# Kernel tuning notes

Measured on AMD Instinct MI355X. Metric: run time of the kernel, lower is better.

The kernel has to match this reference:

```python
import jax, jax.numpy as jnp
import numpy as np

V, E, D = 50000, 800000, 128
EH, NH = 128, 128  # edge_hidden, node_hidden


def setup_inputs() -> dict:
    key = jax.random.key(0)
    ks = jax.random.split(key, 12)
    h = jax.random.normal(ks[0], (V, D), dtype=jnp.float32)
    edge_index = jax.random.randint(ks[1], (2, E), 0, V, dtype=jnp.int64)
    s = 0.02
    # edge MLP: Linear(2D->EH), Linear(EH->EH), Linear(EH->NH)
    W1 = jax.random.normal(ks[2], (2 * D, EH), dtype=jnp.float32) * s
    b1 = jnp.zeros((EH,), dtype=jnp.float32)
    W2 = jax.random.normal(ks[3], (EH, EH), dtype=jnp.float32) * s
    b2 = jnp.zeros((EH,), dtype=jnp.float32)
    W3 = jax.random.normal(ks[4], (EH, NH), dtype=jnp.float32) * s
    b3 = jnp.zeros((NH,), dtype=jnp.float32)
    # node MLP: Linear(D+NH->NH), Linear(NH->NH)
    Wn1 = jax.random.normal(ks[5], (D + NH, NH), dtype=jnp.float32) * s
    bn1 = jnp.zeros((NH,), dtype=jnp.float32)
    Wn2 = jax.random.normal(ks[6], (NH, NH), dtype=jnp.float32) * s
    bn2 = jnp.zeros((NH,), dtype=jnp.float32)
    return {"h": h, "edge_index": edge_index, "W1": W1, "b1": b1, "W2": W2,
            "b2": b2, "W3": W3, "b3": b3, "Wn1": Wn1, "bn1": bn1,
            "Wn2": Wn2, "bn2": bn2}


def reference(h, edge_index, W1, b1, W2, b2, W3, b3, Wn1, bn1, Wn2, bn2):
    src, dst = edge_index[0], edge_index[1]
    # gather node pairs -> edge features (E, 2D)
    edge_feat = jnp.concatenate([h[src], h[dst]], axis=-1)
    # 3-layer edge MLP
    m = jax.nn.relu(edge_feat @ W1 + b1)
    m = jax.nn.relu(m @ W2 + b2)
    messages = m @ W3 + b3                       # (E, NH)
    # scatter-add into destination nodes
    agg = jax.ops.segment_sum(messages, dst, num_segments=h.shape[0])  # (V, NH)
    # node MLP on [h, agg]
    x = jnp.concatenate([h, agg], axis=-1)       # (V, D+NH)
    out = jax.nn.relu(x @ Wn1 + bn1) @ Wn2 + bn2  # (V, NH)
    return out
```

## Files before the change

### kernel.cpp

```cpp
#include <hip/hip_runtime.h>

#define NV 50000
#define NE 800000
#define CVT_N 1600000
#define TR_N  81920
#define W3N_N 16384
#define B3N_N 128
#define NB1 49

typedef _Float16 f16x8 __attribute__((ext_vector_type(8)));
typedef _Float16 f16x4 __attribute__((ext_vector_type(4)));
typedef float    f32x4 __attribute__((ext_vector_type(4)));

static __device__ __forceinline__ f32x4 mfma16(f16x8 a, f16x8 b, f32x4 c) {
  return __builtin_amdgcn_mfma_f32_16x16x32_f16(a, b, c, 0, 0, 0);
}

__global__ void prep_kernel(const float* __restrict__ h, _Float16* __restrict__ hf,
    const float* __restrict__ W1, const float* __restrict__ W2, const float* __restrict__ W3,
    const float* __restrict__ Wn1, const float* __restrict__ Wn2, const float* __restrict__ b3,
    _Float16* __restrict__ w1st, _Float16* __restrict__ w1dt, _Float16* __restrict__ w2t,
    _Float16* __restrict__ wn1c, _Float16* __restrict__ wn2t, float* __restrict__ b3n,
    const int* __restrict__ ei, int* __restrict__ counts)
{
  int i = blockIdx.x * blockDim.x + threadIdx.x;
  if (i < CVT_N) {
    f32x4 v = reinterpret_cast<const f32x4*>(h)[i];
    f16x4 o;
    o[0] = (_Float16)v[0]; o[1] = (_Float16)v[1]; o[2] = (_Float16)v[2]; o[3] = (_Float16)v[3];
    reinterpret_cast<f16x4*>(hf)[i] = o;
    return;
  }
  i -= CVT_N;
  if (i < TR_N) {
    int seg = i >> 14;
    int j = i & 16383;
    int f = j >> 7, k = j & 127;
    switch (seg) {
      case 0: w1st[j] = (_Float16)W1[k * 128 + f]; break;
      case 1: w1dt[j] = (_Float16)W1[(k + 128) * 128 + f]; break;
      case 2: w2t[j]  = (_Float16)W2[k * 128 + f]; break;
      case 3: wn1c[f * 256 + k] = (_Float16)Wn1[k * 128 + f]; break;
      case 4: wn2t[j] = (_Float16)Wn2[k * 128 + f]; break;
    }
    return;
  }
  i -= TR_N;
  if (i < W3N_N) {
    int f = i >> 7, ii = i & 127;
    float a = 0.f;
    for (int j = 0; j < 128; j++) a += W3[ii * 128 + j] * Wn1[(128 + j) * 128 + f];
    wn1c[f * 256 + 128 + ii] = (_Float16)a;
    return;
  }
  i -= W3N_N;
  if (i < B3N_N) {
    float a = 0.f;
    for (int j = 0; j < 128; j++) a += b3[j] * Wn1[(128 + j) * 128 + i];
    b3n[i] = a;
    return;
  }
  i -= B3N_N;
  if (i < NE) atomicAdd(&counts[ei[NE + i]], 1);
}

__global__ __launch_bounds__(1024)
void bsum_kernel(const int* __restrict__ counts, int* __restrict__ bsum) {
  __shared__ int red[1024];
  const int t = threadIdx.x;
  int i = blockIdx.x * 1024 + t;
  red[t] = (i < NV) ? counts[i] : 0;
  __syncthreads();
  for (int off = 512; off > 0; off >>= 1) {
    if (t < off) red[t] += red[t + off];
    __syncthreads();
  }
  if (t == 0) bsum[blockIdx.x] = red[0];
}

__global__ void bscan_kernel(const int* __restrict__ bsum, int* __restrict__ boff) {
  if (threadIdx.x == 0 && blockIdx.x == 0) {
    int run = 0;
    for (int b = 0; b < NB1; b++) { boff[b] = run; run += bsum[b]; }
    boff[NB1] = run;
  }
}

__global__ __launch_bounds__(1024)
void offs_kernel(const int* __restrict__ counts, const int* __restrict__ boff,
                 int* __restrict__ offsets, int* __restrict__ cursor) {
  __shared__ int s[1024];
  const int t = threadIdx.x;
  int i = blockIdx.x * 1024 + t;
  int v = (i < NV) ? counts[i] : 0;
  s[t] = v;
  __syncthreads();
  for (int off = 1; off < 1024; off <<= 1) {
    int x = (t >= off) ? s[t - off] : 0;
    __syncthreads();
    s[t] += x;
    __syncthreads();
  }
  if (i < NV) {
    int excl = boff[blockIdx.x] + s[t] - v;
    offsets[i] = excl;
    cursor[i] = excl;
    if (i == NV - 1) offsets[NV] = boff[blockIdx.x] + s[t];
  }
}

__global__ void permute_kernel(const int* __restrict__ ei, int* __restrict__ cursor,
                               int2* __restrict__ pairs) {
  int e = blockIdx.x * blockDim.x + threadIdx.x;
  if (e < NE) {
    int s = ei[e], d = ei[NE + e];
    int pos = atomicAdd(&cursor[d], 1);
    pairs[pos] = make_int2(s, d);
  }
}

static __device__ __forceinline__ void gemm128_rows(
    const _Float16* __restrict__ hf, const int* nid, const _Float16* __restrict__ At,
    const float* __restrict__ bias, _Float16* __restrict__ Out,
    int nbase, int l15, int quad)
{
  f32x4 acc[8][4];
#pragma unroll
  for (int mt = 0; mt < 8; mt++)
#pragma unroll
    for (int nt = 0; nt < 4; nt++)
      acc[mt][nt] = (f32x4){0.f, 0.f, 0.f, 0.f};

  f16x8 Bc[4], Bn[4];
#pragma unroll
  for (int nt = 0; nt < 4; nt++)
    Bc[nt] = *reinterpret_cast<const f16x8*>(hf + (long long)nid[nt] * 128 + quad * 8);
#pragma unroll
  for (int s = 0; s < 4; s++) {
    if (s < 3) {
#pragma unroll
      for (int nt = 0; nt < 4; nt++)
        Bn[nt] = *reinterpret_cast<const f16x8*>(hf + (long long)nid[nt] * 128 + (s + 1) * 32 + quad * 8);
    }
    const int k = s * 32 + quad * 8;
#pragma unroll
    for (int mt = 0; mt < 8; mt++) {
      f16x8 A = *reinterpret_cast<const f16x8*>(At + (mt * 16 + l15) * 128 + k);
#pragma unroll
      for (int nt = 0; nt < 4; nt++)
        acc[mt][nt] = mfma16(A, Bc[nt], acc[mt][nt]);
    }
#pragma unroll
    for (int nt = 0; nt < 4; nt++) Bc[nt] = Bn[nt];
  }
#pragma unroll
  for (int mt = 0; mt < 8; mt++) {
    f32x4 bb = bias ? *reinterpret_cast<const f32x4*>(bias + mt * 16 + quad * 4)
                    : (f32x4){0.f, 0.f, 0.f, 0.f};
#pragma unroll
    for (int nt = 0; nt < 4; nt++) {
      int n = nbase + nt * 16 + l15;
      if (n < NV) {
        f16x4 o;
#pragma unroll
        for (int r = 0; r < 4; r++) o[r] = (_Float16)(acc[mt][nt][r] + bb[r]);
        *reinterpret_cast<f16x4*>(Out + (long long)n * 128 + mt * 16 + quad * 4) = o;
      }
    }
  }
}

__global__ __launch_bounds__(256, 2)
void h1_kernel(const _Float16* __restrict__ hf, const float* __restrict__ b1,
               const _Float16* __restrict__ w1st, const _Float16* __restrict__ w1dt,
               _Float16* __restrict__ H1s, _Float16* __restrict__ H1d)
{
  const int t = threadIdx.x;
  const int lane = t & 63, wave = t >> 6;
  const int quad = lane >> 4, l15 = lane & 15;
  const int nbase = blockIdx.x * 256 + wave * 64;
  int nid[4];
#pragma unroll
  for (int nt = 0; nt < 4; nt++) {
    int n = nbase + nt * 16 + l15;
    nid[nt] = n < NV ? n : NV - 1;
  }
  if (blockIdx.y == 0) gemm128_rows(hf, nid, w1st, nullptr, H1s, nbase, l15, quad);
  else                 gemm128_rows(hf, nid, w1dt, b1,      H1d, nbase, l15, quad);
}

__global__ __launch_bounds__(128, 3)
void edge_kernel(const _Float16* __restrict__ H1s, const _Float16* __restrict__ H1d,
                 const int2* __restrict__ pairs,
                 const _Float16* __restrict__ w2t, const float* __restrict__ b2,
                 float* __restrict__ agg2)
{
  __shared__ __align__(16) _Float16 M2t[64 * 128];
  __shared__ int segdst[128];
  __shared__ __align__(8) unsigned char sseg8[128];
  __shared__ unsigned long long wmask[2];
  __shared__ int sopen[2];

  const int t = threadIdx.x;
  const int lane = t & 63, wave = t >> 6;
  const int quad = lane >> 4, l15 = lane & 15;
  const int ebase = blockIdx.x * 128;
  const int wbase = wave * 64;

  const int2 prt = pairs[ebase + t];
  if (t == 0)   sopen[0] = (ebase > 0) && (prt.y == pairs[ebase - 1].y);
  if (t == 127) sopen[1] = (ebase + 128 < NE) && (prt.y == pairs[ebase + 128].y);
  const int dprev = (t > 0) ? pairs[ebase + t - 1].y : -1;

  int esrc[4], edst[4];
#pragma unroll
  for (int et = 0; et < 4; et++) {
    int2 pr = pairs[ebase + wbase + et * 16 + l15];
    esrc[et] = pr.x; edst[et] = pr.y;
  }

  f16x8 m1f[4][4];
#pragma unroll
  for (int et = 0; et < 4; et++) {
#pragma unroll
    for (int s = 0; s < 4; s++) {
      f16x8 a = *reinterpret_cast<const f16x8*>(H1s + (long long)esrc[et] * 128 + s * 32 + quad * 8);
      f16x8 b = *reinterpret_cast<const f16x8*>(H1d + (long long)edst[et] * 128 + s * 32 + quad * 8);
      f16x8 o = a + b;
#pragma unroll
      for (int j = 0; j < 8; j++) o[j] = o[j] > (_Float16)0 ? o[j] : (_Float16)0;
      m1f[et][s] = o;
    }
  }

  const bool flag = (t > 0) && (prt.y != dprev);
  unsigned long long bm = __ballot(flag);
  if (lane == 0) wmask[wave] = bm;
  int pre = __popcll(bm & ((1ull << lane) - 1ull)) + (flag ? 1 : 0);
  __syncthreads();
  const int sid = pre + (wave ? (int)__popcll(wmask[0]) : 0);
  sseg8[t] = (unsigned char)sid;
  if (flag || t == 0) segdst[sid] = prt.y;
  const int nseg = (int)__popcll(wmask[0]) + (int)__popcll(wmask[1]) + 1;
  const int nmt = (nseg + 15) >> 4;
  const bool openL = sopen[0] != 0;
  const bool openR = sopen[1] != 0;

  for (int half = 0; half < 2; half++) {
    f32x4 acc[4][4];
#pragma unroll
    for (int et = 0; et < 4; et++)
#pragma unroll
      for (int ft = 0; ft < 4; ft++)
        acc[et][ft] = (f32x4){0.f, 0.f, 0.f, 0.f};

#pragma unroll
    for (int s = 0; s < 4; s++) {
      const int k = s * 32 + quad * 8;
#pragma unroll
      for (int ft = 0; ft < 4; ft++) {
        f16x8 B = *reinterpret_cast<const f16x8*>(w2t + ((half * 4 + ft) * 16 + l15) * 128 + k);
#pragma unroll
        for (int et = 0; et < 4; et++)
          acc[et][ft] = mfma16(m1f[et][s], B, acc[et][ft]);
      }
    }
#pragma unroll
    for (int ft = 0; ft < 4; ft++) {
      const float bv = b2[(half * 4 + ft) * 16 + l15];
#pragma unroll
      for (int et = 0; et < 4; et++) {
        const int g = wave * 16 + et * 4 + quad;
        f16x4 o;
#pragma unroll
        for (int r = 0; r < 4; r++) {
          float x = acc[et][ft][r] + bv;
          o[r] = (_Float16)(x > 0.f ? x : 0.f);
        }
        *reinterpret_cast<f16x4*>(&M2t[(ft * 16 + l15) * 128 + ((g ^ (l15 << 1)) * 4)]) = o;
      }
    }
    __syncthreads();

    f16x8 Bf[2][4];
#pragma unroll
    for (int fl = 0; fl < 2; fl++) {
      const int flr = (wave * 2 + fl) * 16 + l15;
#pragma unroll
      for (int s = 0; s < 4; s++) {
        const int g0 = s * 8 + quad * 2;
        Bf[fl][s] = *reinterpret_cast<const f16x8*>(&M2t[flr * 128 + ((g0 ^ (l15 << 1)) * 4)]);
      }
    }
    unsigned long long segb[4];
#pragma unroll
    for (int s = 0; s < 4; s++)
      segb[s] = *reinterpret_cast<const unsigned long long*>(&sseg8[s * 32 + quad * 8]);
    __syncthreads();

    for (int mt = 0; mt < nmt; mt++) {
      const int myseg = mt * 16 + l15;
      f32x4 racc[2];
#pragma unroll
      for (int fl = 0; fl < 2; fl++) racc[fl] = (f32x4){0.f, 0.f, 0.f, 0.f};
#pragma unroll
      for (int s = 0; s < 4; s++) {
        f16x8 S;
#pragma unroll
        for (int j = 0; j < 8; j++)
          S[j] = ((int)((segb[s] >> (8 * j)) & 255ull) == myseg) ? (_Float16)1 : (_Float16)0;
#pragma unroll
        for (int fl = 0; fl < 2; fl++)
          racc[fl] = mfma16(S, Bf[fl][s], racc[fl]);
      }
#pragma unroll
      for (int fl = 0; fl < 2; fl++) {
        const int f = half * 64 + (wave * 2 + fl) * 16 + l15;
#pragma unroll
        for (int r = 0; r < 4; r++) {
          const int sg = mt * 16 + quad * 4 + r;
          if (sg < nseg) {
            float v = racc[fl][r];
            float* p = agg2 + (long long)segdst[sg] * 128 + f;
            const bool at = (sg == 0 && openL) || (sg == nseg - 1 && openR);
            if (at) unsafeAtomicAdd(p, v); else *p = v;
          }
        }
      }
    }
  }
}

__global__ __launch_bounds__(256, 2)
void node_kernel(const _Float16* __restrict__ hf, const float* __restrict__ agg2,
                 const int* __restrict__ offsets,
                 const _Float16* __restrict__ wn1c, const float* __restrict__ bn1,
                 const float* __restrict__ b3n,
                 const _Float16* __restrict__ wn2t, const float* __restrict__ bn2,
                 float* __restrict__ out)
{
  __shared__ __align__(16) _Float16 M[256 * 128];
  const int t = threadIdx.x;
  const int lane = t & 63, wave = t >> 6;
  const int quad = lane >> 4, l15 = lane & 15;
  const int wbase = wave * 64;
  const int nbase = blockIdx.x * 256 + wbase;

  int nid[4]; float fcnt[4];
#pragma unroll
  for (int nt = 0; nt < 4; nt++) {
    int n = nbase + nt * 16 + l15;
    nid[nt] = n < NV ? n : NV - 1;
    fcnt[nt] = (n < NV) ? (float)(offsets[n + 1] - offsets[n]) : 0.f;
  }

  f32x4 acc[8][4];
#pragma unroll
  for (int mt = 0; mt < 8; mt++)
#pragma unroll
    for (int nt = 0; nt < 4; nt++)
      acc[mt][nt] = (f32x4){0.f, 0.f, 0.f, 0.f};

  f16x8 Bc[4], Bn[4];
#pragma unroll
  for (int nt = 0; nt < 4; nt++)
    Bc[nt] = *reinterpret_cast<const f16x8*>(hf + (long long)nid[nt] * 128 + quad * 8);
#pragma unroll
  for (int s = 0; s < 8; s++) {
    if (s < 7) {
      const int sn = s + 1;
      if (sn < 4) {
#pragma unroll
        for (int nt = 0; nt < 4; nt++)
          Bn[nt] = *reinterpret_cast<const f16x8*>(hf + (long long)nid[nt] * 128 + sn * 32 + quad * 8);
      } else {
#pragma unroll
        for (int nt = 0; nt < 4; nt++) {
          const float* ap = agg2 + (long long)nid[nt] * 128 + (sn - 4) * 32 + quad * 8;
          f32x4 a0 = *reinterpret_cast<const f32x4*>(ap);
          f32x4 a1 = *reinterpret_cast<const f32x4*>(ap + 4);
          f16x8 bb;
#pragma unroll
          for (int j = 0; j < 4; j++) { bb[j] = (_Float16)a0[j]; bb[4 + j] = (_Float16)a1[j]; }
          Bn[nt] = bb;
        }
      }
    }
    const int k = s * 32 + quad * 8;
#pragma unroll
    for (int mt = 0; mt < 8; mt++) {
      f16x8 A = *reinterpret_cast<const f16x8*>(wn1c + (mt * 16 + l15) * 256 + k);
#pragma unroll
      for (int nt = 0; nt < 4; nt++)
        acc[mt][nt] = mfma16(A, Bc[nt], acc[mt][nt]);
    }
#pragma unroll
    for (int nt = 0; nt < 4; nt++) Bc[nt] = Bn[nt];
  }
#pragma unroll
  for (int mt = 0; mt < 8; mt++) {
    f32x4 bb  = *reinterpret_cast<const f32x4*>(bn1 + mt * 16 + quad * 4);
    f32x4 b3c = *reinterpret_cast<const f32x4*>(b3n + mt * 16 + quad * 4);
    const int cbase = 2 * mt + (quad >> 1);
#pragma unroll
    for (int nt = 0; nt < 4; nt++) {
      int row = wbase + nt * 16 + l15;
      int c = cbase ^ (row & 15);
      f16x4 o;
#pragma unroll
      for (int r = 0; r < 4; r++) {
        float x = acc[mt][nt][r] + bb[r] + fcnt[nt] * b3c[r];
        o[r] = (_Float16)(x > 0.f ? x : 0.f);
      }
      *reinterpret_cast<f16x4*>(&M[row * 128 + c * 8 + (quad & 1) * 4]) = o;
      acc[mt][nt] = (f32x4){0.f, 0.f, 0.f, 0.f};
    }
  }

#pragma unroll
  for (int s = 0; s < 4; s++) {
    f16x8 B[4];
#pragma unroll
    for (int nt = 0; nt < 4; nt++) {
      int row = wbase + nt * 16 + l15;
      B[nt] = *reinterpret_cast<const f16x8*>(&M[row * 128 + (((4 * s + quad) ^ (row & 15)) * 8)]);
    }
    const int k = s * 32 + quad * 8;
#pragma unroll
    for (int mt = 0; mt < 8; mt++) {
      f16x8 A = *reinterpret_cast<const f16x8*>(wn2t + (mt * 16 + l15) * 128 + k);
#pragma unroll
      for (int nt = 0; nt < 4; nt++)
        acc[mt][nt] = mfma16(A, B[nt], acc[mt][nt]);
    }
  }
#pragma unroll
  for (int mt = 0; mt < 8; mt++) {
    f32x4 bias = *reinterpret_cast<const f32x4*>(bn2 + mt * 16 + quad * 4);
#pragma unroll
    for (int nt = 0; nt < 4; nt++) {
      int n = nbase + nt * 16 + l15;
      if (n < NV) {
        f32x4 v;
#pragma unroll
        for (int r = 0; r < 4; r++) v[r] = acc[mt][nt][r] + bias[r];
        *reinterpret_cast<f32x4*>(out + (long long)n * 128 + mt * 16 + quad * 4) = v;
      }
    }
  }
}

static inline size_t align16(size_t x) { return (x + 15) & ~(size_t)15; }

extern "C" void kernel_launch(void* const* d_in, const int* in_sizes, int n_in,
                              void* d_out, int out_size, void* d_ws, size_t ws_size,
                              hipStream_t stream)
{
  const float* h   = (const float*)d_in[0];
  const int*   ei  = (const int*)d_in[1];
  const float* W1  = (const float*)d_in[2];
  const float* b1  = (const float*)d_in[3];
  const float* W2  = (const float*)d_in[4];
  const float* b2  = (const float*)d_in[5];
  const float* W3  = (const float*)d_in[6];
  const float* b3  = (const float*)d_in[7];
  const float* Wn1 = (const float*)d_in[8];
  const float* bn1 = (const float*)d_in[9];
  const float* Wn2 = (const float*)d_in[10];
  const float* bn2 = (const float*)d_in[11];
  float* out = (float*)d_out;

  char* p = (char*)d_ws;
  _Float16* hf   = (_Float16*)p; p += align16((size_t)NV * 128 * 2);
  _Float16* H1s  = (_Float16*)p; p += align16((size_t)NV * 128 * 2);
  _Float16* H1d  = (_Float16*)p; p += align16((size_t)NV * 128 * 2);
  _Float16* w1st = (_Float16*)p; p += align16(128 * 128 * 2);
  _Float16* w1dt = (_Float16*)p; p += align16(128 * 128 * 2);
  _Float16* w2t  = (_Float16*)p; p += align16(128 * 128 * 2);
  _Float16* wn1c = (_Float16*)p; p += align16(128 * 256 * 2);
  _Float16* wn2t = (_Float16*)p; p += align16(128 * 128 * 2);
  float*  b3n  = (float*)p;  p += align16(128 * 4);
  int* counts  = (int*)p; p += align16((size_t)NV * 4);
  int* offsets = (int*)p; p += align16((size_t)(NV + 1) * 4);
  int* cursor  = (int*)p; p += align16((size_t)NV * 4);
  int* bsum    = (int*)p; p += align16((size_t)(NB1 + 1) * 4);
  int* boff    = (int*)p; p += align16((size_t)(NB1 + 1) * 4);
  int2* pairs  = (int2*)p; p += align16((size_t)NE * 8);
  float* agg2  = (float*)p; p += align16((size_t)NV * 128 * 4);

  hipMemsetAsync(counts, 0, (size_t)NV * 4, stream);
  hipMemsetAsync(agg2, 0, (size_t)NV * 128 * 4, stream);
  {
    int total = CVT_N + TR_N + W3N_N + B3N_N + NE;
    prep_kernel<<<(total + 255) / 256, 256, 0, stream>>>(
        h, hf, W1, W2, W3, Wn1, Wn2, b3,
        w1st, w1dt, w2t, wn1c, wn2t, b3n, ei, counts);
  }
  bsum_kernel<<<NB1, 1024, 0, stream>>>(counts, bsum);
  bscan_kernel<<<1, 64, 0, stream>>>(bsum, boff);
  offs_kernel<<<NB1, 1024, 0, stream>>>(counts, boff, offsets, cursor);
  permute_kernel<<<(NE + 255) / 256, 256, 0, stream>>>(ei, cursor, pairs);
  h1_kernel<<<dim3((NV + 255) / 256, 2), 256, 0, stream>>>(hf, b1, w1st, w1dt, H1s, H1d);
  edge_kernel<<<NE / 128, 128, 0, stream>>>(H1s, H1d, pairs, w2t, b2, agg2);
  node_kernel<<<(NV + 255) / 256, 256, 0, stream>>>(hf, agg2, offsets, wn1c, bn1, b3n,
                                                    wn2t, bn2, out);
}
```

Measured before the change: 385.7 us.

## Fold block scan into offsets kernel and merge permute with H1 GEMM launch

Removes the single-thread bscan kernel by having each offsets block compute its base with a wave reduction over bsum. It also merges the edge permutation and the H1 GEMM into one launch using block-index partitioning, so the atomic scatter and the MFMA work can run side by side. In edge_kernel, segment-boundary detection now goes through a shared-memory dst array instead of extra global loads, and launch_bounds min-blocks drops from 3 to 2. The aim is fewer launches and better overlap, at the cost of a mixed-workload kernel and possibly lower edge-kernel occupancy.

```diff
diff --git a/kernel.cpp b/kernel.cpp
--- a/kernel.cpp
+++ b/kernel.cpp
@@ -7,6 +7,8 @@
 #define W3N_N 16384
 #define B3N_N 128
 #define NB1 49
+#define NB_PERM 3125
+#define NB_H1 196
 
 typedef _Float16 f16x8 __attribute__((ext_vector_type(8)));
 typedef _Float16 f16x4 __attribute__((ext_vector_type(4)));
@@ -78,22 +80,20 @@
   if (t == 0) bsum[blockIdx.x] = red[0];
 }
 
-__global__ void bscan_kernel(const int* __restrict__ bsum, int* __restrict__ boff) {
-  if (threadIdx.x == 0 && blockIdx.x == 0) {
-    int run = 0;
-    for (int b = 0; b < NB1; b++) { boff[b] = run; run += bsum[b]; }
-    boff[NB1] = run;
-  }
-}
-
 __global__ __launch_bounds__(1024)
-void offs_kernel(const int* __restrict__ counts, const int* __restrict__ boff,
+void offs_kernel(const int* __restrict__ counts, const int* __restrict__ bsum,
                  int* __restrict__ offsets, int* __restrict__ cursor) {
   __shared__ int s[1024];
+  __shared__ int sbase;
   const int t = threadIdx.x;
   int i = blockIdx.x * 1024 + t;
   int v = (i < NV) ? counts[i] : 0;
   s[t] = v;
+  if (t < 64) {
+    int x = (t < blockIdx.x) ? bsum[t] : 0;
+    for (int off = 1; off < 64; off <<= 1) x += __shfl_xor(x, off);
+    if (t == 0) sbase = x;
+  }
   __syncthreads();
   for (int off = 1; off < 1024; off <<= 1) {
     int x = (t >= off) ? s[t - off] : 0;
@@ -102,20 +102,10 @@
     __syncthreads();
   }
   if (i < NV) {
-    int excl = boff[blockIdx.x] + s[t] - v;
+    int excl = sbase + s[t] - v;
     offsets[i] = excl;
     cursor[i] = excl;
-    if (i == NV - 1) offsets[NV] = boff[blockIdx.x] + s[t];
-  }
-}
-
-__global__ void permute_kernel(const int* __restrict__ ei, int* __restrict__ cursor,
-                               int2* __restrict__ pairs) {
-  int e = blockIdx.x * blockDim.x + threadIdx.x;
-  if (e < NE) {
-    int s = ei[e], d = ei[NE + e];
-    int pos = atomicAdd(&cursor[d], 1);
-    pairs[pos] = make_int2(s, d);
+    if (i == NV - 1) offsets[NV] = sbase + s[t];
   }
 }
 
@@ -171,35 +161,49 @@
 }
 
 __global__ __launch_bounds__(256, 2)
-void h1_kernel(const _Float16* __restrict__ hf, const float* __restrict__ b1,
-               const _Float16* __restrict__ w1st, const _Float16* __restrict__ w1dt,
-               _Float16* __restrict__ H1s, _Float16* __restrict__ H1d)
+void h1p_kernel(const _Float16* __restrict__ hf, const float* __restrict__ b1,
+                const _Float16* __restrict__ w1st, const _Float16* __restrict__ w1dt,
+                _Float16* __restrict__ H1s, _Float16* __restrict__ H1d,
+                const int* __restrict__ ei, int* __restrict__ cursor,
+                int2* __restrict__ pairs)
 {
+  int bx = blockIdx.x;
+  if (bx < NB_PERM) {
+    int e = bx * 256 + threadIdx.x;
+    int s = ei[e], d = ei[NE + e];
+    int pos = atomicAdd(&cursor[d], 1);
+    pairs[pos] = make_int2(s, d);
+    return;
+  }
+  bx -= NB_PERM;
+  const int by = bx & 1;
+  const int bxx = bx >> 1;
   const int t = threadIdx.x;
   const int lane = t & 63, wave = t >> 6;
   const int quad = lane >> 4, l15 = lane & 15;
-  const int nbase = blockIdx.x * 256 + wave * 64;
+  const int nbase = bxx * 256 + wave * 64;
   int nid[4];
 #pragma unroll
   for (int nt = 0; nt < 4; nt++) {
     int n = nbase + nt * 16 + l15;
     nid[nt] = n < NV ? n : NV - 1;
   }
-  if (blockIdx.y == 0) gemm128_rows(hf, nid, w1st, nullptr, H1s, nbase, l15, quad);
-  else                 gemm128_rows(hf, nid, w1dt, b1,      H1d, nbase, l15, quad);
-}
-
-__global__ __launch_bounds__(128, 3)
+  if (by == 0) gemm128_rows(hf, nid, w1st, nullptr, H1s, nbase, l15, quad);
+  else         gemm128_rows(hf, nid, w1dt, b1,      H1d, nbase, l15, quad);
+}
+
+__global__ __launch_bounds__(128, 2)
 void edge_kernel(const _Float16* __restrict__ H1s, const _Float16* __restrict__ H1d,
                  const int2* __restrict__ pairs,
                  const _Float16* __restrict__ w2t, const float* __restrict__ b2,
                  float* __restrict__ agg2)
 {
   __shared__ __align__(16) _Float16 M2t[64 * 128];
+  __shared__ int sdst[128];
   __shared__ int segdst[128];
   __shared__ __align__(8) unsigned char sseg8[128];
   __shared__ unsigned long long wmask[2];
-  __shared__ int sopen[2];
+  __shared__ int snbr[2];
 
   const int t = threadIdx.x;
   const int lane = t & 63, wave = t >> 6;
@@ -207,10 +211,9 @@
   const int ebase = blockIdx.x * 128;
   const int wbase = wave * 64;
 
-  const int2 prt = pairs[ebase + t];
-  if (t == 0)   sopen[0] = (ebase > 0) && (prt.y == pairs[ebase - 1].y);
-  if (t == 127) sopen[1] = (ebase + 128 < NE) && (prt.y == pairs[ebase + 128].y);
-  const int dprev = (t > 0) ? pairs[ebase + t - 1].y : -1;
+  { int2 pr = pairs[ebase + t]; sdst[t] = pr.y; }
+  if (t == 0) snbr[0] = (ebase > 0) ? pairs[ebase - 1].y : -1;
+  if (t == 1) snbr[1] = (ebase + 128 < NE) ? pairs[ebase + 128].y : -1;
 
   int esrc[4], edst[4];
 #pragma unroll
@@ -233,18 +236,21 @@
     }
   }
 
-  const bool flag = (t > 0) && (prt.y != dprev);
-  unsigned long long bm = __ballot(flag);
-  if (lane == 0) wmask[wave] = bm;
-  int pre = __popcll(bm & ((1ull << lane) - 1ull)) + (flag ? 1 : 0);
   __syncthreads();
-  const int sid = pre + (wave ? (int)__popcll(wmask[0]) : 0);
-  sseg8[t] = (unsigned char)sid;
-  if (flag || t == 0) segdst[sid] = prt.y;
+  {
+    bool flag = (t > 0) && (sdst[t] != sdst[t - 1]);
+    unsigned long long bm = __ballot(flag);
+    if (lane == 0) wmask[wave] = bm;
+    int pre = __popcll(bm & ((1ull << lane) - 1ull)) + (flag ? 1 : 0);
+    __syncthreads();
+    int sid = pre + (wave ? (int)__popcll(wmask[0]) : 0);
+    sseg8[t] = (unsigned char)sid;
+    if (flag || t == 0) segdst[sid] = sdst[t];
+  }
   const int nseg = (int)__popcll(wmask[0]) + (int)__popcll(wmask[1]) + 1;
   const int nmt = (nseg + 15) >> 4;
-  const bool openL = sopen[0] != 0;
-  const bool openR = sopen[1] != 0;
+  const bool openL = (sdst[0] == snbr[0]);
+  const bool openR = (sdst[127] == snbr[1]);
 
   for (int half = 0; half < 2; half++) {
     f32x4 acc[4][4];
@@ -484,7 +490,6 @@
   int* offsets = (int*)p; p += align16((size_t)(NV + 1) * 4);
   int* cursor  = (int*)p; p += align16((size_t)NV * 4);
   int* bsum    = (int*)p; p += align16((size_t)(NB1 + 1) * 4);
-  int* boff    = (int*)p; p += align16((size_t)(NB1 + 1) * 4);
   int2* pairs  = (int2*)p; p += align16((size_t)NE * 8);
   float* agg2  = (float*)p; p += align16((size_t)NV * 128 * 4);
 
@@ -497,10 +502,9 @@
         w1st, w1dt, w2t, wn1c, wn2t, b3n, ei, counts);
   }
   bsum_kernel<<<NB1, 1024, 0, stream>>>(counts, bsum);
-  bscan_kernel<<<1, 64, 0, stream>>>(bsum, boff);
-  offs_kernel<<<NB1, 1024, 0, stream>>>(counts, boff, offsets, cursor);
-  permute_kernel<<<(NE + 255) / 256, 256, 0, stream>>>(ei, cursor, pairs);
-  h1_kernel<<<dim3((NV + 255) / 256, 2), 256, 0, stream>>>(hf, b1, w1st, w1dt, H1s, H1d);
+  offs_kernel<<<NB1, 1024, 0, stream>>>(counts, bsum, offsets, cursor);
+  h1p_kernel<<<NB_PERM + 2 * NB_H1, 256, 0, stream>>>(hf, b1, w1st, w1dt, H1s, H1d,
+                                                      ei, cursor, pairs);
   edge_kernel<<<NE / 128, 128, 0, stream>>>(H1s, H1d, pairs, w2t, b2, agg2);
   node_kernel<<<(NV + 255) / 256, 256, 0, stream>>>(hf, agg2, offsets, wn1c, bn1, b3n,
                                                     wn2t, bn2, out);
```

Measured after the change: 365.2 us. 5.3% less time.
